# Performance work log

Hardware: AMD Instinct MI355X
Metric: run time of the kernel (lower is better)

The kernel has to match this reference:

```python
import jax, jax.numpy as jnp
import numpy as np

UAV_DIM, TASK_DIM = 32, 32
E, H, HID = 128, 4, 256
B, U, T = 16, 64, 128
ENC_H = 128  # encoder hidden width


def _mlp3(x, w0, b0, w1, b1, w2, b2):
    # Linear->ReLU->Linear->ReLU->Linear (weights stored as (in,out))
    x = jax.nn.relu(x @ w0 + b0)
    x = jax.nn.relu(x @ w1 + b1)
    return x @ w2 + b2


def setup_inputs() -> dict:
    key = jax.random.key(0)
    ks = jax.random.split(key, 20)
    s = lambda fan_in: 1.0 / np.sqrt(fan_in)
    d = {
        'uav_feat': jax.random.normal(ks[0], (B, U, UAV_DIM), jnp.float32),
        'task_feat': jax.random.normal(ks[1], (B, T, TASK_DIM), jnp.float32),
        # UAV encoder
        'uw0': jax.random.normal(ks[2], (UAV_DIM, ENC_H), jnp.float32) * s(UAV_DIM),
        'ub0': jnp.zeros((ENC_H,), jnp.float32),
        'uw1': jax.random.normal(ks[3], (ENC_H, ENC_H), jnp.float32) * s(ENC_H),
        'ub1': jnp.zeros((ENC_H,), jnp.float32),
        'uw2': jax.random.normal(ks[4], (ENC_H, E), jnp.float32) * s(ENC_H),
        'ub2': jnp.zeros((E,), jnp.float32),
        # Task encoder
        'tw0': jax.random.normal(ks[5], (TASK_DIM, ENC_H), jnp.float32) * s(TASK_DIM),
        'tb0': jnp.zeros((ENC_H,), jnp.float32),
        'tw1': jax.random.normal(ks[6], (ENC_H, ENC_H), jnp.float32) * s(ENC_H),
        'tb1': jnp.zeros((ENC_H,), jnp.float32),
        'tw2': jax.random.normal(ks[7], (ENC_H, E), jnp.float32) * s(ENC_H),
        'tb2': jnp.zeros((E,), jnp.float32),
        # head queries + fusion MLP (fw1 is the (2E,HID) first linear)
        'head_q': jax.random.normal(ks[8], (H, E), jnp.float32),
        'fw1': jax.random.normal(ks[9], (2 * E, HID), jnp.float32) * s(2 * E),
        'fb1': jnp.zeros((HID,), jnp.float32),
        'fw2': jax.random.normal(ks[10], (HID, 1), jnp.float32) * s(HID),
        'fb2': jnp.zeros((1,), jnp.float32),
    }
    return d


def reference(uav_feat, task_feat, uw0, ub0, uw1, ub1, uw2, ub2,
              tw0, tb0, tw1, tb1, tw2, tb2, head_q, fw1, fb1, fw2, fb2):
    ue = _mlp3(uav_feat, uw0, ub0, uw1, ub1, uw2, ub2)   # (B,U,E)
    te = _mlp3(task_feat, tw0, tb0, tw1, tb1, tw2, tb2)  # (B,T,E)
    # q = uav_embed + per-head query: (B,H,U,E)
    q = ue[:, None, :, :] + head_q[None, :, None, :]
    # Split cat([q,k]) @ fw1 into q@fw1[:E] + k@fw1[E:] — same math, no 2E concat
    qh = jnp.einsum('bhue,ed->bhud', q, fw1[:E])          # (B,H,U,HID)
    kh = jnp.einsum('bte,ed->btd', te, fw1[E:])           # (B,T,HID)
    pre = qh[:, :, :, None, :] + kh[:, None, None, :, :] + fb1  # (B,H,U,T,HID)
    h = jax.nn.relu(pre)
    logits = jnp.einsum('bhutd,do->bhuto', h, fw2)[..., 0] + fb2[0]  # (B,H,U,T)
    return logits
```

## Files before the change

### kernel.cpp

```cpp
#include <hip/hip_runtime.h>
#include <hip/hip_bf16.h>

#define B_ 16
#define U_ 64
#define T_ 128
#define H_ 4
#define E_ 128
#define HID_ 256

typedef _Float16 half_t;
typedef _Float16 h2 __attribute__((ext_vector_type(2)));
typedef _Float16 f16x8 __attribute__((ext_vector_type(8)));
typedef float f32x4 __attribute__((ext_vector_type(4)));

__device__ __forceinline__ h2 u2h(unsigned u){ h2 r; __builtin_memcpy(&r, &u, 4); return r; }
__device__ __forceinline__ unsigned pkh(float a, float b){
  h2 r; r.x = (_Float16)a; r.y = (_Float16)b;
  unsigned u; __builtin_memcpy(&u, &r, 4); return u;
}

#define PITCH 136
#define PITCH0 40

template<int KC, int SRCN>
__device__ __forceinline__ void stageW(const float* __restrict__ src,
    half_t* __restrict__ dst, int n, int kc0, int pitch)
{
  #pragma unroll
  for (int f=0; f<KC; f++){
    const int kc = kc0 + f;
    float v[8];
    #pragma unroll
    for (int j=0;j<8;j++) v[j] = src[(kc*8+j)*SRCN + n];
    union{ half_t h[8]; uint4 u; } p;
    #pragma unroll
    for (int j=0;j<8;j++) p.h[j] = (half_t)v[j];
    *(uint4*)(dst + n*pitch + kc*8) = p.u;
  }
}

template<int KTILES, int NTILES, int WPITCH, bool RELU>
__device__ __forceinline__ void layer_mfma(const half_t* __restrict__ in,
    const half_t* __restrict__ W, const float* __restrict__ bias,
    half_t* __restrict__ out, int m0, int quad, int l16)
{
  f16x8 bfrag[KTILES];
  const half_t* ip = in + (m0+l16)*PITCH + quad*8;
  #pragma unroll
  for (int kk=0;kk<KTILES;kk++) bfrag[kk] = *(const f16x8*)(ip + kk*32);
  #pragma unroll
  for (int nt=0; nt<NTILES; nt++){
    f32x4 acc = {0.f,0.f,0.f,0.f};
    const half_t* wp = W + (nt*16+l16)*WPITCH + quad*8;
    #pragma unroll
    for (int kk=0;kk<KTILES;kk++){
      f16x8 a = *(const f16x8*)(wp + kk*32);
      acc = __builtin_amdgcn_mfma_f32_16x16x32_f16(a, bfrag[kk], acc, 0, 0, 0);
    }
    const int n0 = nt*16 + quad*4;
    const float4 bv = *(const float4*)(bias + n0);
    float bvr[4] = {bv.x, bv.y, bv.z, bv.w};
    union { half_t h[4]; uint2 u; } pv;
    #pragma unroll
    for (int r=0;r<4;r++){
      float x = acc[r] + bvr[r];
      if (RELU) x = fmaxf(x, 0.f);
      pv.h[r] = (half_t)x;
    }
    *(uint2*)(out + (m0+l16)*PITCH + n0) = pv.u;
  }
}

__global__ __launch_bounds__(256) void enc_mfma(
  const float* __restrict__ uav, const float* __restrict__ task,
  const float* __restrict__ uw0, const float* __restrict__ ub0,
  const float* __restrict__ uw1, const float* __restrict__ ub1,
  const float* __restrict__ uw2, const float* __restrict__ ub2,
  const float* __restrict__ tw0, const float* __restrict__ tb0,
  const float* __restrict__ tw1, const float* __restrict__ tb1,
  const float* __restrict__ tw2, const float* __restrict__ tb2,
  const float* __restrict__ headq, const float* __restrict__ fw1,
  float* __restrict__ ueW, half_t* __restrict__ Kg, float* __restrict__ QhW)
{
  __shared__ half_t W0b[128*PITCH0];
  __shared__ half_t Wb[256*PITCH];
  __shared__ half_t actA[64*PITCH];
  __shared__ half_t actB[64*PITCH];
  const int tid = threadIdx.x;

  if (blockIdx.x == 48) {
    const int n = tid;
    float acc[4] = {0.f,0.f,0.f,0.f};
    for (int e=0;e<128;e++){
      float w = fw1[e*256 + n];
      #pragma unroll
      for (int h=0;h<4;h++) acc[h] = fmaf(headq[h*128+e], w, acc[h]);
    }
    #pragma unroll
    for (int h=0;h<4;h++) QhW[h*256+n] = acc[h];
    return;
  }

  const int lane = tid&63, wv = tid>>6;
  const int quad = lane>>4, l16 = lane&15;
  const int m0 = wv*16;
  const bool isU = blockIdx.x < 16;
  const int rows0 = (isU ? blockIdx.x : blockIdx.x - 16) * 64;
  const float* Xsrc = (isU ? uav : task) + rows0*32;
  const float* W0 = isU ? uw0 : tw0;
  const float* W1 = isU ? uw1 : tw1;
  const float* W2 = isU ? uw2 : tw2;
  const float* W3 = fw1 + (isU ? 0 : 128*HID_);
  const float* bias0 = isU ? ub0 : tb0;
  const float* bias1 = isU ? ub1 : tb1;
  const float* bias2 = isU ? ub2 : tb2;

  const int tn = tid & 127, th = tid >> 7;

  {
    const int r = tid>>2, q = tid&3;
    const float4 v0 = *(const float4*)(Xsrc + r*32 + q*8);
    const float4 v1 = *(const float4*)(Xsrc + r*32 + q*8 + 4);
    union{ half_t h[8]; uint4 u; } p;
    p.h[0]=(half_t)v0.x; p.h[1]=(half_t)v0.y; p.h[2]=(half_t)v0.z; p.h[3]=(half_t)v0.w;
    p.h[4]=(half_t)v1.x; p.h[5]=(half_t)v1.y; p.h[6]=(half_t)v1.z; p.h[7]=(half_t)v1.w;
    *(uint4*)(actA + r*PITCH + q*8) = p.u;
  }
  stageW<2,128>(W0, W0b, tn, th*2, PITCH0);
  stageW<8,128>(W1, Wb,            tn, th*8, PITCH);
  stageW<8,128>(W2, Wb + 128*PITCH,tn, th*8, PITCH);
  __syncthreads();

  layer_mfma<1,8,PITCH0,true >(actA, W0b,          bias0, actB, m0, quad, l16);
  layer_mfma<4,8,PITCH, true >(actB, Wb,           bias1, actA, m0, quad, l16);
  __syncthreads();
  stageW<8,256>(W3, Wb, tn, th*8, PITCH);
  layer_mfma<4,8,PITCH, false>(actA, Wb+128*PITCH, bias2, actB, m0, quad, l16);
  __syncthreads();
  stageW<8,256>(W3, Wb, 128 + tn, th*8, PITCH);
  __syncthreads();

  {
    f16x8 bfrag[4];
    const half_t* ip = actB + (m0+l16)*PITCH + quad*8;
    #pragma unroll
    for (int kk=0;kk<4;kk++) bfrag[kk] = *(const f16x8*)(ip + kk*32);
    const int grow = rows0 + m0 + l16;
    #pragma unroll
    for (int nt=0; nt<16; nt++){
      f32x4 acc = {0.f,0.f,0.f,0.f};
      const half_t* wp = Wb + (nt*16+l16)*PITCH + quad*8;
      #pragma unroll
      for (int kk=0;kk<4;kk++){
        f16x8 a = *(const f16x8*)(wp + kk*32);
        acc = __builtin_amdgcn_mfma_f32_16x16x32_f16(a, bfrag[kk], acc, 0, 0, 0);
      }
      const int n0 = nt*16 + quad*4;
      if (isU){
        *(float4*)(ueW + grow*256 + n0) = make_float4(acc[0],acc[1],acc[2],acc[3]);
      } else {
        union { half_t h[4]; uint2 u; } pv;
        pv.h[0]=(half_t)acc[0]; pv.h[1]=(half_t)acc[1];
        pv.h[2]=(half_t)acc[2]; pv.h[3]=(half_t)acc[3];
        *(uint2*)(Kg + grow*256 + n0) = pv.u;
      }
    }
  }
}

#define UTILE 8

__global__ __launch_bounds__(256) void logits_kernel(
  const float* __restrict__ ueW, const float* __restrict__ QhW,
  const half_t* __restrict__ Kg,
  const float* __restrict__ fb1, const float* __restrict__ fw2,
  const float* __restrict__ fb2, float* __restrict__ out)
{
  __shared__ uint4 Kl4[128*32];
  __shared__ uint4 baseb[UTILE][32];
  __shared__ uint4 w2b[32];

  const int tid = threadIdx.x;
  const int b = blockIdx.z, h = blockIdx.y;
  const int u0 = blockIdx.x * UTILE;

  {
    const int u = tid >> 5;
    const int c = tid & 31;
    const float4* ue4 = (const float4*)(ueW + (b*U_ + u0 + u)*HID_);
    const float4* q4  = (const float4*)(QhW + h*HID_);
    const float4* f4  = (const float4*)fb1;
    float4 a0 = ue4[2*c],   a1 = ue4[2*c+1];
    float4 b0 = q4[2*c],    b1 = q4[2*c+1];
    float4 c0 = f4[2*c],    c1 = f4[2*c+1];
    uint4 pv;
    pv.x = pkh(a0.x+b0.x+c0.x, a0.y+b0.y+c0.y);
    pv.y = pkh(a0.z+b0.z+c0.z, a0.w+b0.w+c0.w);
    pv.z = pkh(a1.x+b1.x+c1.x, a1.y+b1.y+c1.y);
    pv.w = pkh(a1.z+b1.z+c1.z, a1.w+b1.w+c1.w);
    baseb[u][c] = pv;
    if (tid < 32) {
      const float4* w4 = (const float4*)fw2;
      float4 w0 = w4[2*tid], w1 = w4[2*tid+1];
      uint4 wv4;
      wv4.x = pkh(w0.x, w0.y); wv4.y = pkh(w0.z, w0.w);
      wv4.z = pkh(w1.x, w1.y); wv4.w = pkh(w1.z, w1.w);
      w2b[tid] = wv4;
    }
  }
  const uint4* Kgp = (const uint4*)(Kg + (size_t)b*T_*HID_);
  #pragma unroll
  for (int i = tid; i < 128*32; i += 256){
    const int t = i >> 5, c = i & 31;
    Kl4[t*32 + ((c + t)&31)] = Kgp[t*32 + c];
  }
  __syncthreads();

  const int wv = tid >> 6, lane = tid & 63;
  const int r0 = (wv & 1) * 4;
  const int t  = (wv >> 1) * 64 + lane;
  const float fb2f = fb2[0];
  const uint4* myrow = Kl4 + t*32;
  const h2 hz = (h2)((_Float16)0);

  float acc[4] = {0.f,0.f,0.f,0.f};
  #pragma unroll
  for (int c=0; c<32; c++){
    const uint4 kv = myrow[(c + t)&31];
    const uint4 w4 = w2b[c];
    #pragma unroll
    for (int r=0; r<4; r++){
      const uint4 p = baseb[r0+r][c];
      h2 x;
      x = __builtin_elementwise_max(u2h(p.x)+u2h(kv.x), hz);
      acc[r] = __builtin_amdgcn_fdot2(x, u2h(w4.x), acc[r], false);
      x = __builtin_elementwise_max(u2h(p.y)+u2h(kv.y), hz);
      acc[r] = __builtin_amdgcn_fdot2(x, u2h(w4.y), acc[r], false);
      x = __builtin_elementwise_max(u2h(p.z)+u2h(kv.z), hz);
      acc[r] = __builtin_amdgcn_fdot2(x, u2h(w4.z), acc[r], false);
      x = __builtin_elementwise_max(u2h(p.w)+u2h(kv.w), hz);
      acc[r] = __builtin_amdgcn_fdot2(x, u2h(w4.w), acc[r], false);
    }
  }
  #pragma unroll
  for (int r=0; r<4; r++)
    out[((b*H_ + h)*U_ + (u0 + r0 + r))*T_ + t] = acc[r] + fb2f;
}

extern "C" void kernel_launch(void* const* d_in, const int* in_sizes, int n_in,
                              void* d_out, int out_size, void* d_ws, size_t ws_size,
                              hipStream_t stream)
{
  const float* uav  = (const float*)d_in[0];
  const float* task = (const float*)d_in[1];
  const float* uw0=(const float*)d_in[2];  const float* ub0=(const float*)d_in[3];
  const float* uw1=(const float*)d_in[4];  const float* ub1=(const float*)d_in[5];
  const float* uw2=(const float*)d_in[6];  const float* ub2=(const float*)d_in[7];
  const float* tw0=(const float*)d_in[8];  const float* tb0=(const float*)d_in[9];
  const float* tw1=(const float*)d_in[10]; const float* tb1=(const float*)d_in[11];
  const float* tw2=(const float*)d_in[12]; const float* tb2=(const float*)d_in[13];
  const float* headq=(const float*)d_in[14];
  const float* fw1=(const float*)d_in[15];
  const float* fb1=(const float*)d_in[16];
  const float* fw2=(const float*)d_in[17];
  const float* fb2=(const float*)d_in[18];

  float* ueW = (float*)d_ws;
  float* QhW = ueW + 262144;
  half_t* Kg = (half_t*)(QhW + 1024);

  float* out = (float*)d_out;

  hipLaunchKernelGGL(enc_mfma, dim3(49), dim3(256), 0, stream,
      uav, task, uw0, ub0, uw1, ub1, uw2, ub2,
      tw0, tb0, tw1, tb1, tw2, tb2, headq, fw1,
      ueW, Kg, QhW);
  hipLaunchKernelGGL(logits_kernel, dim3(U_/UTILE, H_, B_), dim3(256), 0, stream,
      ueW, QhW, Kg, fb1, fw2, fb2, out);
}
```

Before: 113.3 us.

## Precompute per-head fp16 base rows in encoder and stream them in logits kernel

The encoder's UAV blocks now compute headq@fw1+fb1 themselves and write fully combined fp16 base rows per (b,h,u), replacing the separate fp32 ueW and QhW buffers. The logits kernel no longer builds the base tile in shared memory; it reads base and fw2 directly from global memory (uniform, cached loads) and stages K with a padded pitch instead of a rotated index. This drops a prologue, a sync dependency and fp32 traffic, but every UAV block now redundantly recomputes the head-query projection, and the base workspace grows by a factor of H in fp16.

```diff
diff --git a/kernel.cpp b/kernel.cpp
--- a/kernel.cpp
+++ b/kernel.cpp
@@ -14,13 +14,10 @@
 typedef float f32x4 __attribute__((ext_vector_type(4)));
 
 __device__ __forceinline__ h2 u2h(unsigned u){ h2 r; __builtin_memcpy(&r, &u, 4); return r; }
-__device__ __forceinline__ unsigned pkh(float a, float b){
-  h2 r; r.x = (_Float16)a; r.y = (_Float16)b;
-  unsigned u; __builtin_memcpy(&u, &r, 4); return u;
-}
 
 #define PITCH 136
 #define PITCH0 40
+#define KPITCH 33
 
 template<int KC, int SRCN>
 __device__ __forceinline__ void stageW(const float* __restrict__ src,
@@ -80,26 +77,17 @@
   const float* __restrict__ tw1, const float* __restrict__ tb1,
   const float* __restrict__ tw2, const float* __restrict__ tb2,
   const float* __restrict__ headq, const float* __restrict__ fw1,
-  float* __restrict__ ueW, half_t* __restrict__ Kg, float* __restrict__ QhW)
+  const float* __restrict__ fb1, const float* __restrict__ fw2,
+  half_t* __restrict__ baseg, half_t* __restrict__ Kg, half_t* __restrict__ w2h)
 {
   __shared__ half_t W0b[128*PITCH0];
   __shared__ half_t Wb[256*PITCH];
   __shared__ half_t actA[64*PITCH];
   __shared__ half_t actB[64*PITCH];
+  __shared__ float  qf[4][256];
   const int tid = threadIdx.x;
 
-  if (blockIdx.x == 48) {
-    const int n = tid;
-    float acc[4] = {0.f,0.f,0.f,0.f};
-    for (int e=0;e<128;e++){
-      float w = fw1[e*256 + n];
-      #pragma unroll
-      for (int h=0;h<4;h++) acc[h] = fmaf(headq[h*128+e], w, acc[h]);
-    }
-    #pragma unroll
-    for (int h=0;h<4;h++) QhW[h*256+n] = acc[h];
-    return;
-  }
+  if (blockIdx.x == 48) { w2h[tid] = (half_t)fw2[tid]; return; }
 
   const int lane = tid&63, wv = tid>>6;
   const int quad = lane>>4, l16 = lane&15;
@@ -127,8 +115,23 @@
     *(uint4*)(actA + r*PITCH + q*8) = p.u;
   }
   stageW<2,128>(W0, W0b, tn, th*2, PITCH0);
-  stageW<8,128>(W1, Wb,            tn, th*8, PITCH);
-  stageW<8,128>(W2, Wb + 128*PITCH,tn, th*8, PITCH);
+  stageW<8,128>(W1, Wb,             tn, th*8, PITCH);
+  stageW<8,128>(W2, Wb + 128*PITCH, tn, th*8, PITCH);
+
+  if (isU){
+    const int n = tid;
+    float fb = fb1[n];
+    float q0=fb, q1=fb, q2=fb, q3=fb;
+    #pragma unroll 8
+    for (int e=0;e<128;e++){
+      float w = fw1[e*256 + n];
+      q0 = fmaf(headq[      e], w, q0);
+      q1 = fmaf(headq[128 + e], w, q1);
+      q2 = fmaf(headq[256 + e], w, q2);
+      q3 = fmaf(headq[384 + e], w, q3);
+    }
+    qf[0][n]=q0; qf[1][n]=q1; qf[2][n]=q2; qf[3][n]=q3;
+  }
   __syncthreads();
 
   layer_mfma<1,8,PITCH0,true >(actA, W0b,          bias0, actB, m0, quad, l16);
@@ -145,7 +148,8 @@
     const half_t* ip = actB + (m0+l16)*PITCH + quad*8;
     #pragma unroll
     for (int kk=0;kk<4;kk++) bfrag[kk] = *(const f16x8*)(ip + kk*32);
-    const int grow = rows0 + m0 + l16;
+    const int urow = m0 + l16;
+    const int grow = rows0 + urow;
     #pragma unroll
     for (int nt=0; nt<16; nt++){
       f32x4 acc = {0.f,0.f,0.f,0.f};
@@ -157,80 +161,62 @@
       }
       const int n0 = nt*16 + quad*4;
       if (isU){
-        *(float4*)(ueW + grow*256 + n0) = make_float4(acc[0],acc[1],acc[2],acc[3]);
+        const int b = blockIdx.x;
+        #pragma unroll
+        for (int h=0;h<4;h++){
+          const float4 qv = *(const float4*)(&qf[h][n0]);
+          union { half_t hh[4]; uint2 u; } pv;
+          pv.hh[0]=(half_t)(acc[0]+qv.x); pv.hh[1]=(half_t)(acc[1]+qv.y);
+          pv.hh[2]=(half_t)(acc[2]+qv.z); pv.hh[3]=(half_t)(acc[3]+qv.w);
+          *(uint2*)(baseg + ((size_t)((b*H_ + h)*U_ + urow))*HID_ + n0) = pv.u;
+        }
       } else {
-        union { half_t h[4]; uint2 u; } pv;
-        pv.h[0]=(half_t)acc[0]; pv.h[1]=(half_t)acc[1];
-        pv.h[2]=(half_t)acc[2]; pv.h[3]=(half_t)acc[3];
-        *(uint2*)(Kg + grow*256 + n0) = pv.u;
+        union { half_t hh[4]; uint2 u; } pv;
+        pv.hh[0]=(half_t)acc[0]; pv.hh[1]=(half_t)acc[1];
+        pv.hh[2]=(half_t)acc[2]; pv.hh[3]=(half_t)acc[3];
+        *(uint2*)(Kg + (size_t)grow*HID_ + n0) = pv.u;
       }
     }
   }
 }
 
-#define UTILE 8
-
 __global__ __launch_bounds__(256) void logits_kernel(
-  const float* __restrict__ ueW, const float* __restrict__ QhW,
-  const half_t* __restrict__ Kg,
-  const float* __restrict__ fb1, const float* __restrict__ fw2,
-  const float* __restrict__ fb2, float* __restrict__ out)
-{
-  __shared__ uint4 Kl4[128*32];
-  __shared__ uint4 baseb[UTILE][32];
-  __shared__ uint4 w2b[32];
+  const half_t* __restrict__ baseg, const half_t* __restrict__ Kg,
+  const half_t* __restrict__ w2h, const float* __restrict__ fb2,
+  float* __restrict__ out)
+{
+  __shared__ uint4 Kl[128*KPITCH];
 
   const int tid = threadIdx.x;
   const int b = blockIdx.z, h = blockIdx.y;
-  const int u0 = blockIdx.x * UTILE;
-
-  {
-    const int u = tid >> 5;
-    const int c = tid & 31;
-    const float4* ue4 = (const float4*)(ueW + (b*U_ + u0 + u)*HID_);
-    const float4* q4  = (const float4*)(QhW + h*HID_);
-    const float4* f4  = (const float4*)fb1;
-    float4 a0 = ue4[2*c],   a1 = ue4[2*c+1];
-    float4 b0 = q4[2*c],    b1 = q4[2*c+1];
-    float4 c0 = f4[2*c],    c1 = f4[2*c+1];
-    uint4 pv;
-    pv.x = pkh(a0.x+b0.x+c0.x, a0.y+b0.y+c0.y);
-    pv.y = pkh(a0.z+b0.z+c0.z, a0.w+b0.w+c0.w);
-    pv.z = pkh(a1.x+b1.x+c1.x, a1.y+b1.y+c1.y);
-    pv.w = pkh(a1.z+b1.z+c1.z, a1.w+b1.w+c1.w);
-    baseb[u][c] = pv;
-    if (tid < 32) {
-      const float4* w4 = (const float4*)fw2;
-      float4 w0 = w4[2*tid], w1 = w4[2*tid+1];
-      uint4 wv4;
-      wv4.x = pkh(w0.x, w0.y); wv4.y = pkh(w0.z, w0.w);
-      wv4.z = pkh(w1.x, w1.y); wv4.w = pkh(w1.z, w1.w);
-      w2b[tid] = wv4;
-    }
-  }
+  const int u0 = blockIdx.x * 8;
+
   const uint4* Kgp = (const uint4*)(Kg + (size_t)b*T_*HID_);
   #pragma unroll
   for (int i = tid; i < 128*32; i += 256){
-    const int t = i >> 5, c = i & 31;
-    Kl4[t*32 + ((c + t)&31)] = Kgp[t*32 + c];
-  }
-  __syncthreads();
-
-  const int wv = tid >> 6, lane = tid & 63;
-  const int r0 = (wv & 1) * 4;
-  const int t  = (wv >> 1) * 64 + lane;
+    const int t = i >> 5, cc = i & 31;
+    Kl[t*KPITCH + cc] = Kgp[i];
+  }
+  __syncthreads();
+
+  const int wvu = __builtin_amdgcn_readfirstlane(tid >> 6);
+  const int lane = tid & 63;
+  const int r0 = (wvu & 1) * 4;
+  const int t  = (wvu >> 1) * 64 + lane;
+  const uint4* myrow = Kl + t*KPITCH;
+  const uint4* bp = (const uint4*)(baseg + ((size_t)((b*H_ + h)*U_ + u0 + r0))*HID_);
+  const uint4* wp = (const uint4*)w2h;
   const float fb2f = fb2[0];
-  const uint4* myrow = Kl4 + t*32;
   const h2 hz = (h2)((_Float16)0);
 
   float acc[4] = {0.f,0.f,0.f,0.f};
-  #pragma unroll
+  #pragma unroll 4
   for (int c=0; c<32; c++){
-    const uint4 kv = myrow[(c + t)&31];
-    const uint4 w4 = w2b[c];
+    const uint4 kv = myrow[c];
+    const uint4 w4 = wp[c];
     #pragma unroll
     for (int r=0; r<4; r++){
-      const uint4 p = baseb[r0+r][c];
+      const uint4 p = bp[r*32 + c];
       h2 x;
       x = __builtin_elementwise_max(u2h(p.x)+u2h(kv.x), hz);
       acc[r] = __builtin_amdgcn_fdot2(x, u2h(w4.x), acc[r], false);
@@ -265,16 +251,16 @@
   const float* fw2=(const float*)d_in[17];
   const float* fb2=(const float*)d_in[18];
 
-  float* ueW = (float*)d_ws;
-  float* QhW = ueW + 262144;
-  half_t* Kg = (half_t*)(QhW + 1024);
+  half_t* baseg = (half_t*)d_ws;
+  half_t* Kg    = baseg + (size_t)B_*H_*U_*HID_;
+  half_t* w2h   = Kg + (size_t)B_*T_*HID_;
 
   float* out = (float*)d_out;
 
   hipLaunchKernelGGL(enc_mfma, dim3(49), dim3(256), 0, stream,
       uav, task, uw0, ub0, uw1, ub1, uw2, ub2,
-      tw0, tb0, tw1, tb1, tw2, tb2, headq, fw1,
-      ueW, Kg, QhW);
-  hipLaunchKernelGGL(logits_kernel, dim3(U_/UTILE, H_, B_), dim3(256), 0, stream,
-      ueW, QhW, Kg, fb1, fw2, fb2, out);
-}
+      tw0, tb0, tw1, tb1, tw2, tb2, headq, fw1, fb1, fw2,
+      baseg, Kg, w2h);
+  hipLaunchKernelGGL(logits_kernel, dim3(U_/8, H_, B_), dim3(256), 0, stream,
+      baseg, Kg, w2h, fb2, out);
+}
```

After: 122.9 us. +8.5%, slower.

## Split encoder rows across twice as many blocks with N-split waves

Applied to the files above, without the earlier changes.

The encoder kernel now handles 32 rows per block instead of 64, doubling the grid from 49 to 97 blocks. Within a block, the four waves are arranged as 2 row tiles × 2 output-column halves. This spreads the small encoder over more compute units to cut its latency. The cost is that each block re-stages the full weight matrices, which doubles global weight reads and conversion work, and an extra barrier is needed between layers.

```diff
diff --git a/kernel.cpp b/kernel.cpp
--- a/kernel.cpp
+++ b/kernel.cpp
@@ -39,17 +39,18 @@
   }
 }
 
-template<int KTILES, int NTILES, int WPITCH, bool RELU>
-__device__ __forceinline__ void layer_mfma(const half_t* __restrict__ in,
+template<int KTILES, int NT, int WPITCH, bool RELU>
+__device__ __forceinline__ void layer_ns(const half_t* __restrict__ in,
     const half_t* __restrict__ W, const float* __restrict__ bias,
-    half_t* __restrict__ out, int m0, int quad, int l16)
+    half_t* __restrict__ out, int m0, int nt0, int quad, int l16)
 {
   f16x8 bfrag[KTILES];
   const half_t* ip = in + (m0+l16)*PITCH + quad*8;
   #pragma unroll
   for (int kk=0;kk<KTILES;kk++) bfrag[kk] = *(const f16x8*)(ip + kk*32);
   #pragma unroll
-  for (int nt=0; nt<NTILES; nt++){
+  for (int j=0; j<NT; j++){
+    const int nt = nt0 + j;
     f32x4 acc = {0.f,0.f,0.f,0.f};
     const half_t* wp = W + (nt*16+l16)*WPITCH + quad*8;
     #pragma unroll
@@ -84,11 +85,11 @@
 {
   __shared__ half_t W0b[128*PITCH0];
   __shared__ half_t Wb[256*PITCH];
-  __shared__ half_t actA[64*PITCH];
-  __shared__ half_t actB[64*PITCH];
+  __shared__ half_t actA[32*PITCH];
+  __shared__ half_t actB[32*PITCH];
   const int tid = threadIdx.x;
 
-  if (blockIdx.x == 48) {
+  if (blockIdx.x == 96) {
     const int n = tid;
     float acc[4] = {0.f,0.f,0.f,0.f};
     for (int e=0;e<128;e++){
@@ -103,9 +104,10 @@
 
   const int lane = tid&63, wv = tid>>6;
   const int quad = lane>>4, l16 = lane&15;
-  const int m0 = wv*16;
-  const bool isU = blockIdx.x < 16;
-  const int rows0 = (isU ? blockIdx.x : blockIdx.x - 16) * 64;
+  const int tr = wv & 1, nh = wv >> 1;
+  const int m0 = tr*16;
+  const bool isU = blockIdx.x < 32;
+  const int rows0 = (isU ? blockIdx.x : blockIdx.x - 32) * 32;
   const float* Xsrc = (isU ? uav : task) + rows0*32;
   const float* W0 = isU ? uw0 : tw0;
   const float* W1 = isU ? uw1 : tw1;
@@ -117,7 +119,7 @@
 
   const int tn = tid & 127, th = tid >> 7;
 
-  {
+  if (tid < 128){
     const int r = tid>>2, q = tid&3;
     const float4 v0 = *(const float4*)(Xsrc + r*32 + q*8);
     const float4 v1 = *(const float4*)(Xsrc + r*32 + q*8 + 4);
@@ -127,15 +129,16 @@
     *(uint4*)(actA + r*PITCH + q*8) = p.u;
   }
   stageW<2,128>(W0, W0b, tn, th*2, PITCH0);
-  stageW<8,128>(W1, Wb,            tn, th*8, PITCH);
-  stageW<8,128>(W2, Wb + 128*PITCH,tn, th*8, PITCH);
-  __syncthreads();
-
-  layer_mfma<1,8,PITCH0,true >(actA, W0b,          bias0, actB, m0, quad, l16);
-  layer_mfma<4,8,PITCH, true >(actB, Wb,           bias1, actA, m0, quad, l16);
+  stageW<8,128>(W1, Wb,             tn, th*8, PITCH);
+  stageW<8,128>(W2, Wb + 128*PITCH, tn, th*8, PITCH);
+  __syncthreads();
+
+  layer_ns<1,4,PITCH0,true >(actA, W0b,          bias0, actB, m0, nh*4, quad, l16);
+  __syncthreads();
+  layer_ns<4,4,PITCH, true >(actB, Wb,           bias1, actA, m0, nh*4, quad, l16);
   __syncthreads();
   stageW<8,256>(W3, Wb, tn, th*8, PITCH);
-  layer_mfma<4,8,PITCH, false>(actA, Wb+128*PITCH, bias2, actB, m0, quad, l16);
+  layer_ns<4,4,PITCH, false>(actA, Wb+128*PITCH, bias2, actB, m0, nh*4, quad, l16);
   __syncthreads();
   stageW<8,256>(W3, Wb, 128 + tn, th*8, PITCH);
   __syncthreads();
@@ -147,7 +150,8 @@
     for (int kk=0;kk<4;kk++) bfrag[kk] = *(const f16x8*)(ip + kk*32);
     const int grow = rows0 + m0 + l16;
     #pragma unroll
-    for (int nt=0; nt<16; nt++){
+    for (int j=0; j<8; j++){
+      const int nt = nh*8 + j;
       f32x4 acc = {0.f,0.f,0.f,0.f};
       const half_t* wp = Wb + (nt*16+l16)*PITCH + quad*8;
       #pragma unroll
@@ -159,10 +163,10 @@
       if (isU){
         *(float4*)(ueW + grow*256 + n0) = make_float4(acc[0],acc[1],acc[2],acc[3]);
       } else {
-        union { half_t h[4]; uint2 u; } pv;
-        pv.h[0]=(half_t)acc[0]; pv.h[1]=(half_t)acc[1];
-        pv.h[2]=(half_t)acc[2]; pv.h[3]=(half_t)acc[3];
-        *(uint2*)(Kg + grow*256 + n0) = pv.u;
+        union { half_t hh[4]; uint2 u; } pv;
+        pv.hh[0]=(half_t)acc[0]; pv.hh[1]=(half_t)acc[1];
+        pv.hh[2]=(half_t)acc[2]; pv.hh[3]=(half_t)acc[3];
+        *(uint2*)(Kg + (size_t)grow*HID_ + n0) = pv.u;
       }
     }
   }
@@ -271,7 +275,7 @@
 
   float* out = (float*)d_out;
 
-  hipLaunchKernelGGL(enc_mfma, dim3(49), dim3(256), 0, stream,
+  hipLaunchKernelGGL(enc_mfma, dim3(97), dim3(256), 0, stream,
       uav, task, uw0, ub0, uw1, ub1, uw2, ub2,
       tw0, tb0, tw1, tb1, tw2, tb2, headq, fw1,
       ueW, Kg, QhW);
```

Result: no change. 112.7 us (median of 2 runs) (-0.5%).
